# Kernel optimization log

Hardware: AMD Instinct MI355X
Metric: run time of the kernel (lower is better)

## Reference

```python
import jax, jax.numpy as jnp
import numpy as np

N_NODES = 50000
N_EDGES = 800000
NODE_DIM = 32
EDGE_DIM = 16
HIDDEN = 64


def setup_inputs() -> dict:
    key = jax.random.key(0)
    ks = jax.random.split(key, 7)
    h = jax.random.normal(ks[0], (N_NODES, HIDDEN), dtype=jnp.float32)
    nf = jax.random.normal(ks[1], (N_NODES, NODE_DIM), dtype=jnp.float32)
    ef = jax.random.normal(ks[2], (N_EDGES, EDGE_DIM), dtype=jnp.float32)
    src = jax.random.randint(ks[3], (N_EDGES,), 0, N_NODES, dtype=jnp.int32)
    dst = jax.random.randint(ks[4], (N_EDGES,), 0, N_NODES, dtype=jnp.int32)
    # torch Linear weights: [out_features, in_features]
    in1 = HIDDEN + 2 * NODE_DIM + EDGE_DIM  # 144
    W1 = jax.random.normal(ks[5], (HIDDEN, in1), dtype=jnp.float32) * (1.0 / np.sqrt(in1))
    W2 = jax.random.normal(ks[6], (HIDDEN, HIDDEN), dtype=jnp.float32) * (1.0 / np.sqrt(HIDDEN))
    return {"h": h, "nf": nf, "ef": ef, "src": src, "dst": dst, "W1": W1, "W2": W2}


def reference(h, nf, ef, src, dst, W1, W2):
    n = nf.shape[0]
    # per-edge message: concat(dst.x, edge.x, src.h)  -> [E, node+edge+hidden]
    m_e = jnp.concatenate([nf[dst], ef, h[src]], axis=-1)
    # mailbox sum per destination node
    m = jax.ops.segment_sum(m_e, dst, num_segments=n)  # [N, node+edge+hidden]
    z = jnp.concatenate([nf, m], axis=-1)              # [N, hidden+2*node+edge]
    new_h = jax.nn.relu(z @ W1.T) @ W2.T               # [N, hidden]
    # DGL update_all only updates nodes that received at least one message
    deg = jax.ops.segment_sum(jnp.ones_like(dst, dtype=jnp.float32), dst, num_segments=n)
    return jnp.where(deg[:, None] > 0, new_h, h)
```

## Files before the change

### kernel.cpp

```cpp
#include <hip/hip_runtime.h>

#define NDIM 32
#define EDIM 16
#define NHID 64
#define NIN1 144
#define SCHUNK 1024
#define SPT 4
#define SBLK 128
#define HB 8

__device__ __forceinline__ unsigned pk2(float a, float b) {
  unsigned ua = __float_as_uint(a);
  unsigned ub = __float_as_uint(b);
  ua = (ua + 0x7FFFu + ((ua >> 16) & 1u)) >> 16;
  ub = (ub + 0x7FFFu + ((ub >> 16) & 1u)) >> 16;
  return ua | (ub << 16);
}
__device__ __forceinline__ float lo16(unsigned u) { return __uint_as_float(u << 16); }
__device__ __forceinline__ float hi16(unsigned u) { return __uint_as_float(u & 0xFFFF0000u); }

#define ACC8(A, V)                                   \
  do {                                               \
    A[0] += lo16((V).x); A[1] += hi16((V).x);        \
    A[2] += lo16((V).y); A[3] += hi16((V).y);        \
    A[4] += lo16((V).z); A[5] += hi16((V).z);        \
    A[6] += lo16((V).w); A[7] += hi16((V).w);        \
  } while (0)

__global__ __launch_bounds__(256) void sse_hist(
    const int* __restrict__ dst, int* __restrict__ counts,
    int* __restrict__ rank,
    const float* __restrict__ W1, float* __restrict__ W1T,
    const float* __restrict__ W2, float* __restrict__ W2T,
    const float* __restrict__ h, uint4* __restrict__ h16,
    int E, int N, int eblocks) {
  int b = blockIdx.x;
  if (b < eblocks) {
    int ebase = b * (256 * HB) + threadIdx.x;
    int r[HB];
#pragma unroll
    for (int i = 0; i < HB; ++i) {
      int e = ebase + i * 256;
      if (e < E) r[i] = atomicAdd(&counts[dst[e]], 1);
    }
#pragma unroll
    for (int i = 0; i < HB; ++i) {
      int e = ebase + i * 256;
      if (e < E) rank[e] = r[i];
    }
  } else {
    int t = (b - eblocks) * 256 + threadIdx.x;
    int T = SBLK * 256;
    if (t < NHID * NIN1) {
      int rr = t / NIN1, k = t - rr * NIN1;
      W1T[k * NHID + rr] = W1[t];
    } else if (t < NHID * NIN1 + NHID * NHID) {
      int i = t - NHID * NIN1;
      int rr = i >> 6, k = i & 63;
      W2T[k * NHID + rr] = W2[i];
    }
    const float4* hf4 = (const float4*)h;
    int NH = N * 8;
    for (int i = t; i < NH; i += T) {
      float4 x = hf4[2 * i], y = hf4[2 * i + 1];
      uint4 o;
      o.x = pk2(x.x, x.y); o.y = pk2(x.z, x.w);
      o.z = pk2(y.x, y.y); o.w = pk2(y.z, y.w);
      h16[i] = o;
    }
  }
}

__global__ __launch_bounds__(256) void sse_scan_part(
    const int* __restrict__ counts, int* __restrict__ bsum, int N) {
  __shared__ int ws[4];
  int t = threadIdx.x;
  int base = blockIdx.x * SCHUNK + t * SPT;
  int s = 0;
#pragma unroll
  for (int i = 0; i < SPT; ++i) {
    int idx = base + i;
    if (idx < N) s += counts[idx];
  }
  int v = s;
#pragma unroll
  for (int off = 1; off < 64; off <<= 1) v += __shfl_xor(v, off, 64);
  if ((t & 63) == 0) ws[t >> 6] = v;
  __syncthreads();
  if (t == 0) bsum[blockIdx.x] = ws[0] + ws[1] + ws[2] + ws[3];
}

__global__ __launch_bounds__(256) void sse_scan_final(
    const int* __restrict__ counts, const int* __restrict__ bsum,
    int* __restrict__ starts, int N, int nb) {
  __shared__ int ws[4];
  int t = threadIdx.x;
  int lane = t & 63, w = t >> 6;
  int boff = 0;
  for (int j = 0; j < (int)blockIdx.x; ++j) boff += bsum[j];
  int base = blockIdx.x * SCHUNK + t * SPT;
  int c[SPT];
  int s = 0;
#pragma unroll
  for (int i = 0; i < SPT; ++i) {
    int idx = base + i;
    c[i] = (idx < N) ? counts[idx] : 0;
    s += c[i];
  }
  int incl = s;
#pragma unroll
  for (int off = 1; off < 64; off <<= 1) {
    int u = __shfl_up(incl, off, 64);
    if (lane >= off) incl += u;
  }
  if (lane == 63) ws[w] = incl;
  __syncthreads();
  int woff = 0;
#pragma unroll
  for (int j = 0; j < 4; ++j)
    if (j < w) woff += ws[j];
  int run = boff + woff + (incl - s);
#pragma unroll
  for (int i = 0; i < SPT; ++i) {
    int idx = base + i;
    if (idx < N) {
      starts[idx] = run;
      run += c[i];
    }
  }
  if ((int)blockIdx.x == nb - 1 && t == 0)
    starts[N] = boff + ws[0] + ws[1] + ws[2] + ws[3];
}

__global__ __launch_bounds__(256) void sse_build(
    const int* __restrict__ src, const int* __restrict__ dst,
    const int* __restrict__ rank, const int* __restrict__ starts,
    int2* __restrict__ sedge, int E) {
  int ebase = blockIdx.x * 1024 + threadIdx.x;
#pragma unroll
  for (int i = 0; i < 4; ++i) {
    int e = ebase + i * 256;
    if (e < E) {
      int d = dst[e];
      int pos = starts[d] + rank[e];
      sedge[pos] = make_int2(src[e], e);
    }
  }
}

__global__ __launch_bounds__(256) void sse_gather(
    const uint4* __restrict__ h16, const float* __restrict__ ef,
    const int2* __restrict__ sedge, const int* __restrict__ starts,
    uint4* __restrict__ efsum16, uint4* __restrict__ hsum16, int N) {
  int w = threadIdx.x >> 6;
  int lane = threadIdx.x & 63;
  int node = blockIdx.x * 4 + w;
  if (node >= N) return;
  int st = starts[node], en = starts[node + 1];

  const float4* ef4 = (const float4*)ef;
  int q8 = lane >> 3, m = lane & 7;
  int eq = lane >> 2, em = lane & 3;

  float acc[8];
#pragma unroll
  for (int i = 0; i < 8; ++i) acc[i] = 0.f;
  float4 ea = make_float4(0.f, 0.f, 0.f, 0.f);

  for (int base = st; base < en; base += 64) {
    int C = en - base; C = C > 64 ? 64 : C;
    int2 seg = (lane < C) ? sedge[base + lane] : make_int2(0, 0);
    int myS = seg.x, myE = seg.y;
    int nr = (C + 31) >> 5;
    for (int r = 0; r < nr; ++r) {
      int b = r * 32;
      int i0 = b + q8, i1 = b + 8 + q8, i2 = b + 16 + q8, i3 = b + 24 + q8;
      int s0 = __shfl(myS, i0, 64);
      int s1 = __shfl(myS, i1, 64);
      int s2 = __shfl(myS, i2, 64);
      int s3 = __shfl(myS, i3, 64);
      int e0 = b + eq, e1 = b + 16 + eq;
      int id0 = __shfl(myE, e0, 64);
      int id1 = __shfl(myE, e1, 64);
      uint4 v0 = h16[(size_t)s0 * 8 + m];
      uint4 v1 = h16[(size_t)s1 * 8 + m];
      uint4 v2 = h16[(size_t)s2 * 8 + m];
      uint4 v3 = h16[(size_t)s3 * 8 + m];
      float4 x0 = ef4[(size_t)id0 * 4 + em];
      float4 x1 = ef4[(size_t)id1 * 4 + em];
      if (i0 < C) ACC8(acc, v0);
      if (i1 < C) ACC8(acc, v1);
      if (i2 < C) ACC8(acc, v2);
      if (i3 < C) ACC8(acc, v3);
      if (e0 < C) { ea.x += x0.x; ea.y += x0.y; ea.z += x0.z; ea.w += x0.w; }
      if (e1 < C) { ea.x += x1.x; ea.y += x1.y; ea.z += x1.z; ea.w += x1.w; }
    }
  }

#pragma unroll
  for (int off = 8; off < 64; off <<= 1)
#pragma unroll
    for (int i = 0; i < 8; ++i) acc[i] += __shfl_xor(acc[i], off, 64);
  if (lane < 8) {
    uint4 o;
    o.x = pk2(acc[0], acc[1]); o.y = pk2(acc[2], acc[3]);
    o.z = pk2(acc[4], acc[5]); o.w = pk2(acc[6], acc[7]);
    hsum16[(size_t)node * 8 + lane] = o;
  }
#pragma unroll
  for (int off = 4; off < 64; off <<= 1) {
    ea.x += __shfl_xor(ea.x, off, 64);
    ea.y += __shfl_xor(ea.y, off, 64);
    ea.z += __shfl_xor(ea.z, off, 64);
    ea.w += __shfl_xor(ea.w, off, 64);
  }
  float bx = __shfl_xor(ea.x, 1, 64);
  float by = __shfl_xor(ea.y, 1, 64);
  float bz = __shfl_xor(ea.z, 1, 64);
  float bw = __shfl_xor(ea.w, 1, 64);
  if (lane < 4 && (lane & 1) == 0) {
    uint4 o;
    o.x = pk2(ea.x, ea.y); o.y = pk2(ea.z, ea.w);
    o.z = pk2(bx, by);     o.w = pk2(bz, bw);
    efsum16[(size_t)node * 2 + (lane >> 1)] = o;
  }
}

__global__ __launch_bounds__(256) void sse_node(
    const float* __restrict__ h, const float* __restrict__ nf,
    const uint4* __restrict__ efsum16, const uint4* __restrict__ hsum16,
    const int* __restrict__ starts, const float* __restrict__ W1T,
    const float* __restrict__ W2T, float* __restrict__ out, int N) {
  __shared__ float4 zs[36 * 64];
  __shared__ float4 as[16 * 64];

  int tid = threadIdx.x;
  int lane = tid & 63;
  int w = __builtin_amdgcn_readfirstlane(tid) >> 6;

  int node = blockIdx.x * 64 + lane;
  int nodeC = node < N ? node : N - 1;

  if (w == 0) {
    int st = starts[nodeC], en = starts[nodeC + 1];
    float dg = (float)(en - st);
    const float4* nfr = (const float4*)(nf + (size_t)nodeC * NDIM);
#pragma unroll
    for (int k4 = 0; k4 < 8; ++k4) {
      float4 v = nfr[k4];
      zs[k4 * 64 + lane] = v;
      zs[(8 + k4) * 64 + lane] =
          make_float4(dg * v.x, dg * v.y, dg * v.z, dg * v.w);
    }
  } else if (w == 1) {
    uint4 a = efsum16[(size_t)nodeC * 2 + 0];
    uint4 b = efsum16[(size_t)nodeC * 2 + 1];
    zs[16 * 64 + lane] = make_float4(lo16(a.x), hi16(a.x), lo16(a.y), hi16(a.y));
    zs[17 * 64 + lane] = make_float4(lo16(a.z), hi16(a.z), lo16(a.w), hi16(a.w));
    zs[18 * 64 + lane] = make_float4(lo16(b.x), hi16(b.x), lo16(b.y), hi16(b.y));
    zs[19 * 64 + lane] = make_float4(lo16(b.z), hi16(b.z), lo16(b.w), hi16(b.w));
  } else if (w == 2) {
#pragma unroll
    for (int c = 0; c < 4; ++c) {
      uint4 u = hsum16[(size_t)nodeC * 8 + c];
      zs[(20 + 2 * c) * 64 + lane] =
          make_float4(lo16(u.x), hi16(u.x), lo16(u.y), hi16(u.y));
      zs[(21 + 2 * c) * 64 + lane] =
          make_float4(lo16(u.z), hi16(u.z), lo16(u.w), hi16(u.w));
    }
  } else {
#pragma unroll
    for (int c = 4; c < 8; ++c) {
      uint4 u = hsum16[(size_t)nodeC * 8 + c];
      zs[(20 + 2 * c) * 64 + lane] =
          make_float4(lo16(u.x), hi16(u.x), lo16(u.y), hi16(u.y));
      zs[(21 + 2 * c) * 64 + lane] =
          make_float4(lo16(u.z), hi16(u.z), lo16(u.w), hi16(u.w));
    }
  }
  __syncthreads();

  const float4* w1b = (const float4*)W1T + w * 4;
  float a[16];
#pragma unroll
  for (int j = 0; j < 16; ++j) a[j] = 0.f;

#pragma unroll 2
  for (int k4 = 0; k4 < 36; ++k4) {
    float4 zv = zs[k4 * 64 + lane];
#pragma unroll
    for (int kk = 0; kk < 4; ++kk) {
      int k = k4 * 4 + kk;
      float4 w0 = w1b[k * 16 + 0];
      float4 w1 = w1b[k * 16 + 1];
      float4 w2 = w1b[k * 16 + 2];
      float4 w3 = w1b[k * 16 + 3];
      float zk = kk == 0 ? zv.x : kk == 1 ? zv.y : kk == 2 ? zv.z : zv.w;
      a[0]  = fmaf(w0.x, zk, a[0]);
      a[1]  = fmaf(w0.y, zk, a[1]);
      a[2]  = fmaf(w0.z, zk, a[2]);
      a[3]  = fmaf(w0.w, zk, a[3]);
      a[4]  = fmaf(w1.x, zk, a[4]);
      a[5]  = fmaf(w1.y, zk, a[5]);
      a[6]  = fmaf(w1.z, zk, a[6]);
      a[7]  = fmaf(w1.w, zk, a[7]);
      a[8]  = fmaf(w2.x, zk, a[8]);
      a[9]  = fmaf(w2.y, zk, a[9]);
      a[10] = fmaf(w2.z, zk, a[10]);
      a[11] = fmaf(w2.w, zk, a[11]);
      a[12] = fmaf(w3.x, zk, a[12]);
      a[13] = fmaf(w3.y, zk, a[13]);
      a[14] = fmaf(w3.z, zk, a[14]);
      a[15] = fmaf(w3.w, zk, a[15]);
    }
  }

#pragma unroll
  for (int j4 = 0; j4 < 4; ++j4)
    as[(w * 4 + j4) * 64 + lane] =
        make_float4(fmaxf(a[j4 * 4 + 0], 0.f), fmaxf(a[j4 * 4 + 1], 0.f),
                    fmaxf(a[j4 * 4 + 2], 0.f), fmaxf(a[j4 * 4 + 3], 0.f));
  __syncthreads();

  const float4* w2b = (const float4*)W2T + w * 4;
  float o[16];
#pragma unroll
  for (int j = 0; j < 16; ++j) o[j] = 0.f;

#pragma unroll 2
  for (int kq = 0; kq < 16; ++kq) {
    float4 av = as[kq * 64 + lane];
#pragma unroll
    for (int kk = 0; kk < 4; ++kk) {
      int k = kq * 4 + kk;
      float4 w0 = w2b[k * 16 + 0];
      float4 w1 = w2b[k * 16 + 1];
      float4 w2 = w2b[k * 16 + 2];
      float4 w3 = w2b[k * 16 + 3];
      float ak = kk == 0 ? av.x : kk == 1 ? av.y : kk == 2 ? av.z : av.w;
      o[0]  = fmaf(w0.x, ak, o[0]);
      o[1]  = fmaf(w0.y, ak, o[1]);
      o[2]  = fmaf(w0.z, ak, o[2]);
      o[3]  = fmaf(w0.w, ak, o[3]);
      o[4]  = fmaf(w1.x, ak, o[4]);
      o[5]  = fmaf(w1.y, ak, o[5]);
      o[6]  = fmaf(w1.z, ak, o[6]);
      o[7]  = fmaf(w1.w, ak, o[7]);
      o[8]  = fmaf(w2.x, ak, o[8]);
      o[9]  = fmaf(w2.y, ak, o[9]);
      o[10] = fmaf(w2.z, ak, o[10]);
      o[11] = fmaf(w2.w, ak, o[11]);
      o[12] = fmaf(w3.x, ak, o[12]);
      o[13] = fmaf(w3.y, ak, o[13]);
      o[14] = fmaf(w3.z, ak, o[14]);
      o[15] = fmaf(w3.w, ak, o[15]);
    }
  }

  if (node < N) {
    int st = starts[node], en = starts[node + 1];
    float4* o4 = (float4*)(out + (size_t)node * NHID + w * 16);
    if (en - st == 0) {
      const float4* hr = (const float4*)(h + (size_t)node * NHID + w * 16);
#pragma unroll
      for (int j4 = 0; j4 < 4; ++j4) o4[j4] = hr[j4];
    } else {
#pragma unroll
      for (int j4 = 0; j4 < 4; ++j4)
        o4[j4] = make_float4(o[j4 * 4 + 0], o[j4 * 4 + 1], o[j4 * 4 + 2],
                             o[j4 * 4 + 3]);
    }
  }
}

extern "C" void kernel_launch(void* const* d_in, const int* in_sizes, int n_in,
                              void* d_out, int out_size, void* d_ws, size_t ws_size,
                              hipStream_t stream) {
  const float* h  = (const float*)d_in[0];
  const float* nf = (const float*)d_in[1];
  const float* ef = (const float*)d_in[2];
  const int*   src = (const int*)d_in[3];
  const int*   dst = (const int*)d_in[4];
  const float* W1 = (const float*)d_in[5];
  const float* W2 = (const float*)d_in[6];
  float* out = (float*)d_out;

  int N = in_sizes[0] / NHID;
  int E = in_sizes[3];

  char* p = (char*)d_ws;
  int2* sedge = (int2*)p;                 p += (size_t)E * 8;
  int* counts = (int*)p;                  p += (size_t)N * 4;
  int* starts = (int*)p;                  p += (size_t)(N + 1) * 4;
  int* bsum = (int*)p;                    p += 64 * 4;
  float* W1T = (float*)p;                 p += (size_t)NIN1 * NHID * 4;
  float* W2T = (float*)p;                 p += (size_t)NHID * NHID * 4;
  p = (char*)(((size_t)p + 15) & ~(size_t)15);
  uint4* h16 = (uint4*)p;                 p += (size_t)N * 128;
  uint4* efsum16 = (uint4*)p;             p += (size_t)N * 32;
  uint4* hsum16 = (uint4*)p;              p += (size_t)N * 128;
  int* rank = (int*)hsum16;

  hipMemsetAsync(counts, 0, (size_t)N * sizeof(int), stream);

  int eblocks8 = (E + 256 * HB - 1) / (256 * HB);
  int eblocks4 = (E + 1023) / 1024;
  int nb = (N + SCHUNK - 1) / SCHUNK;

  sse_hist<<<eblocks8 + SBLK, 256, 0, stream>>>(dst, counts, rank, W1, W1T,
                                                W2, W2T, h, h16, E, N,
                                                eblocks8);
  sse_scan_part<<<nb, 256, 0, stream>>>(counts, bsum, N);
  sse_scan_final<<<nb, 256, 0, stream>>>(counts, bsum, starts, N, nb);
  sse_build<<<eblocks4, 256, 0, stream>>>(src, dst, rank, starts, sedge, E);

  int gblocks = (N + 3) / 4;
  sse_gather<<<gblocks, 256, 0, stream>>>(h16, ef, sedge, starts,
                                          efsum16, hsum16, N);

  int nblocks = (N + 63) / 64;
  sse_node<<<nblocks, 256, 0, stream>>>(h, nf, efsum16, hsum16, starts, W1T,
                                        W2T, out, N);
}
```

Measured before the change: 225.8 us.

## Split gather into two column-half passes and widen build per-thread edges

The single per-node gather kernel becomes two kernels. The first sums the lower half of the bf16 h row (4 lanes × 16B) together with edge features, and the second sums the upper half of h. Each pass touches a smaller slice of the h16 table, which may improve cache locality for the random gathers, at the cost of re-reading the sorted edge list and launching one more kernel. The build kernel also processes 8 edges per thread instead of 4.

Result: slower. 245.8 us (+8.8%).

```diff
diff --git a/kernel.cpp b/kernel.cpp
--- a/kernel.cpp
+++ b/kernel.cpp
@@ -8,6 +8,7 @@
 #define SPT 4
 #define SBLK 128
 #define HB 8
+#define BB 8
 
 __device__ __forceinline__ unsigned pk2(float a, float b) {
   unsigned ua = __float_as_uint(a);
@@ -136,9 +137,9 @@
     const int* __restrict__ src, const int* __restrict__ dst,
     const int* __restrict__ rank, const int* __restrict__ starts,
     int2* __restrict__ sedge, int E) {
-  int ebase = blockIdx.x * 1024 + threadIdx.x;
-#pragma unroll
-  for (int i = 0; i < 4; ++i) {
+  int ebase = blockIdx.x * (256 * BB) + threadIdx.x;
+#pragma unroll
+  for (int i = 0; i < BB; ++i) {
     int e = ebase + i * 256;
     if (e < E) {
       int d = dst[e];
@@ -148,7 +149,7 @@
   }
 }
 
-__global__ __launch_bounds__(256) void sse_gather(
+__global__ __launch_bounds__(256) void sse_gather_h0ef(
     const uint4* __restrict__ h16, const float* __restrict__ ef,
     const int2* __restrict__ sedge, const int* __restrict__ starts,
     uint4* __restrict__ efsum16, uint4* __restrict__ hsum16, int N) {
@@ -159,8 +160,7 @@
   int st = starts[node], en = starts[node + 1];
 
   const float4* ef4 = (const float4*)ef;
-  int q8 = lane >> 3, m = lane & 7;
-  int eq = lane >> 2, em = lane & 3;
+  int q4 = lane >> 2, m = lane & 3;
 
   float acc[8];
 #pragma unroll
@@ -174,34 +174,27 @@
     int nr = (C + 31) >> 5;
     for (int r = 0; r < nr; ++r) {
       int b = r * 32;
-      int i0 = b + q8, i1 = b + 8 + q8, i2 = b + 16 + q8, i3 = b + 24 + q8;
+      int i0 = b + q4, i1 = b + 16 + q4;
       int s0 = __shfl(myS, i0, 64);
       int s1 = __shfl(myS, i1, 64);
-      int s2 = __shfl(myS, i2, 64);
-      int s3 = __shfl(myS, i3, 64);
-      int e0 = b + eq, e1 = b + 16 + eq;
-      int id0 = __shfl(myE, e0, 64);
-      int id1 = __shfl(myE, e1, 64);
+      int id0 = __shfl(myE, i0, 64);
+      int id1 = __shfl(myE, i1, 64);
       uint4 v0 = h16[(size_t)s0 * 8 + m];
       uint4 v1 = h16[(size_t)s1 * 8 + m];
-      uint4 v2 = h16[(size_t)s2 * 8 + m];
-      uint4 v3 = h16[(size_t)s3 * 8 + m];
-      float4 x0 = ef4[(size_t)id0 * 4 + em];
-      float4 x1 = ef4[(size_t)id1 * 4 + em];
+      float4 x0 = ef4[(size_t)id0 * 4 + m];
+      float4 x1 = ef4[(size_t)id1 * 4 + m];
       if (i0 < C) ACC8(acc, v0);
       if (i1 < C) ACC8(acc, v1);
-      if (i2 < C) ACC8(acc, v2);
-      if (i3 < C) ACC8(acc, v3);
-      if (e0 < C) { ea.x += x0.x; ea.y += x0.y; ea.z += x0.z; ea.w += x0.w; }
-      if (e1 < C) { ea.x += x1.x; ea.y += x1.y; ea.z += x1.z; ea.w += x1.w; }
-    }
-  }
-
-#pragma unroll
-  for (int off = 8; off < 64; off <<= 1)
+      if (i0 < C) { ea.x += x0.x; ea.y += x0.y; ea.z += x0.z; ea.w += x0.w; }
+      if (i1 < C) { ea.x += x1.x; ea.y += x1.y; ea.z += x1.z; ea.w += x1.w; }
+    }
+  }
+
+#pragma unroll
+  for (int off = 4; off < 64; off <<= 1)
 #pragma unroll
     for (int i = 0; i < 8; ++i) acc[i] += __shfl_xor(acc[i], off, 64);
-  if (lane < 8) {
+  if (lane < 4) {
     uint4 o;
     o.x = pk2(acc[0], acc[1]); o.y = pk2(acc[2], acc[3]);
     o.z = pk2(acc[4], acc[5]); o.w = pk2(acc[6], acc[7]);
@@ -223,6 +216,52 @@
     o.x = pk2(ea.x, ea.y); o.y = pk2(ea.z, ea.w);
     o.z = pk2(bx, by);     o.w = pk2(bz, bw);
     efsum16[(size_t)node * 2 + (lane >> 1)] = o;
+  }
+}
+
+__global__ __launch_bounds__(256) void sse_gather_h1(
+    const uint4* __restrict__ h16, const int2* __restrict__ sedge,
+    const int* __restrict__ starts, uint4* __restrict__ hsum16, int N) {
+  int w = threadIdx.x >> 6;
+  int lane = threadIdx.x & 63;
+  int node = blockIdx.x * 4 + w;
+  if (node >= N) return;
+  int st = starts[node], en = starts[node + 1];
+
+  int q4 = lane >> 2, m = lane & 3;
+
+  float acc[8];
+#pragma unroll
+  for (int i = 0; i < 8; ++i) acc[i] = 0.f;
+
+  for (int base = st; base < en; base += 64) {
+    int C = en - base; C = C > 64 ? 64 : C;
+    int2 seg = (lane < C) ? sedge[base + lane] : make_int2(0, 0);
+    int myS = seg.x;
+    int i0 = q4, i1 = 16 + q4, i2 = 32 + q4, i3 = 48 + q4;
+    int s0 = __shfl(myS, i0, 64);
+    int s1 = __shfl(myS, i1, 64);
+    int s2 = __shfl(myS, i2, 64);
+    int s3 = __shfl(myS, i3, 64);
+    uint4 v0 = h16[(size_t)s0 * 8 + 4 + m];
+    uint4 v1 = h16[(size_t)s1 * 8 + 4 + m];
+    uint4 v2 = h16[(size_t)s2 * 8 + 4 + m];
+    uint4 v3 = h16[(size_t)s3 * 8 + 4 + m];
+    if (i0 < C) ACC8(acc, v0);
+    if (i1 < C) ACC8(acc, v1);
+    if (i2 < C) ACC8(acc, v2);
+    if (i3 < C) ACC8(acc, v3);
+  }
+
+#pragma unroll
+  for (int off = 4; off < 64; off <<= 1)
+#pragma unroll
+    for (int i = 0; i < 8; ++i) acc[i] += __shfl_xor(acc[i], off, 64);
+  if (lane < 4) {
+    uint4 o;
+    o.x = pk2(acc[0], acc[1]); o.y = pk2(acc[2], acc[3]);
+    o.z = pk2(acc[4], acc[5]); o.w = pk2(acc[6], acc[7]);
+    hsum16[(size_t)node * 8 + 4 + lane] = o;
   }
 }
 
@@ -404,7 +443,7 @@
   hipMemsetAsync(counts, 0, (size_t)N * sizeof(int), stream);
 
   int eblocks8 = (E + 256 * HB - 1) / (256 * HB);
-  int eblocks4 = (E + 1023) / 1024;
+  int bblocks  = (E + 256 * BB - 1) / (256 * BB);
   int nb = (N + SCHUNK - 1) / SCHUNK;
 
   sse_hist<<<eblocks8 + SBLK, 256, 0, stream>>>(dst, counts, rank, W1, W1T,
@@ -412,11 +451,12 @@
                                                 eblocks8);
   sse_scan_part<<<nb, 256, 0, stream>>>(counts, bsum, N);
   sse_scan_final<<<nb, 256, 0, stream>>>(counts, bsum, starts, N, nb);
-  sse_build<<<eblocks4, 256, 0, stream>>>(src, dst, rank, starts, sedge, E);
+  sse_build<<<bblocks, 256, 0, stream>>>(src, dst, rank, starts, sedge, E);
 
   int gblocks = (N + 3) / 4;
-  sse_gather<<<gblocks, 256, 0, stream>>>(h16, ef, sedge, starts,
-                                          efsum16, hsum16, N);
+  sse_gather_h0ef<<<gblocks, 256, 0, stream>>>(h16, ef, sedge, starts,
+                                               efsum16, hsum16, N);
+  sse_gather_h1<<<gblocks, 256, 0, stream>>>(h16, sedge, starts, hsum16, N);
 
   int nblocks = (N + 63) / 64;
   sse_node<<<nblocks, 256, 0, stream>>>(h, nf, efsum16, hsum16, starts, W1T,
```
